# Kernel tuning notes

Hardware: AMD Instinct MI355X
Metric: run time of the kernel (lower is better)

Reference implementation:

```python
import jax, jax.numpy as jnp
import numpy as np

NUM_NODES = 100000
NODE_FEAT_DIM = 512
EDGE_FEAT_DIM = 512
MEM_DIM = NODE_FEAT_DIM + EDGE_FEAT_DIM  # 1024
BATCH = 65536


def setup_inputs() -> dict:
    key = jax.random.key(0)
    k_ids, k_mem, k_emb, kq, ks, kk = jax.random.split(key, 6)
    scale = 1.0 / np.sqrt(MEM_DIM)
    inp = {
        "node_ids": jax.random.randint(k_ids, (BATCH,), 0, NUM_NODES, dtype=jnp.int64)
        if jax.config.jax_enable_x64 else
        jax.random.randint(k_ids, (BATCH,), 0, NUM_NODES, dtype=jnp.int32),
        # memory bank: (N, 1, D); randomized (instead of the zero init) so math is non-trivial
        "node_memories": jax.random.normal(k_mem, (NUM_NODES, 1, MEM_DIM), dtype=jnp.float32) * 0.02,
        "node_embedding": jax.random.normal(k_emb, (NUM_NODES, MEM_DIM), dtype=jnp.float32) * 0.02,
        "Wq": jax.random.normal(jax.random.fold_in(kq, 0), (MEM_DIM, NODE_FEAT_DIM), dtype=jnp.float32) * scale,
        "bq": jnp.zeros((NODE_FEAT_DIM,), dtype=jnp.float32),
        "Ws": jax.random.normal(jax.random.fold_in(ks, 0), (MEM_DIM, NODE_FEAT_DIM), dtype=jnp.float32) * scale,
        "bs": jnp.zeros((NODE_FEAT_DIM,), dtype=jnp.float32),
        "Wk": jax.random.normal(jax.random.fold_in(kk, 0), (MEM_DIM, NODE_FEAT_DIM), dtype=jnp.float32) * scale,
        "bk": jnp.zeros((NODE_FEAT_DIM,), dtype=jnp.float32),
    }
    return inp


def reference(node_ids, node_memories, node_embedding, Wq, bq, Ws, bs, Wk, bk):
    ids = node_ids.astype(jnp.int32)
    # torch.sum(node_memories[ids], dim=2): reduces feature dim -> (B, 1)
    mem_sum = jnp.sum(node_memories[ids], axis=2)          # (B, 1)
    x = mem_sum + node_embedding[ids]                      # broadcast -> (B, D)
    q = jax.nn.sigmoid(x @ Wq + bq)                        # (B, node_feat_dim)
    s = jax.nn.sigmoid(x @ Ws + bs)
    k = jax.nn.sigmoid(x @ Wk + bk)
    return (q, s, k)
```

## Files before the change

### kernel.cpp

```cpp
#include <hip/hip_runtime.h>
#include <hip/hip_bf16.h>
#include <stdint.h>

#define BATCH_N 65536
#define KDIM 1024
#define NTOT 1536

typedef __bf16 bf16x8 __attribute__((ext_vector_type(8)));
typedef float f32x4 __attribute__((ext_vector_type(4)));

__device__ __forceinline__ unsigned short f2bf(float f) {
    unsigned u = __builtin_bit_cast(unsigned, f);
    u += 0x7FFFu + ((u >> 16) & 1u);
    return (unsigned short)(u >> 16);
}

__global__ __launch_bounds__(256) void prep_kernel(
    const int* __restrict__ ids,
    const float* __restrict__ mem,
    const float* __restrict__ emb,
    unsigned short* __restrict__ x)
{
    const int b    = blockIdx.x * 4 + (threadIdx.x >> 6);
    const int lane = threadIdx.x & 63;
    const int id   = ids[b];
    const float4* m4 = (const float4*)(mem + (size_t)id * KDIM) + lane;
    const float4* e4 = (const float4*)(emb + (size_t)id * KDIM) + lane;
    float4 v0 = m4[0];
    float4 v1 = m4[64];
    float4 v2 = m4[128];
    float4 v3 = m4[192];
    float s = (v0.x + v0.y + v0.z + v0.w) + (v1.x + v1.y + v1.z + v1.w)
            + (v2.x + v2.y + v2.z + v2.w) + (v3.x + v3.y + v3.z + v3.w);
    #pragma unroll
    for (int off = 1; off < 64; off <<= 1) s += __shfl_xor(s, off, 64);
    unsigned short* xb = x + (size_t)b * KDIM;
    #pragma unroll
    for (int q = 0; q < 4; ++q) {
        float4 e = e4[q * 64];
        ushort4 o;
        o.x = f2bf(s + e.x);
        o.y = f2bf(s + e.y);
        o.z = f2bf(s + e.z);
        o.w = f2bf(s + e.w);
        const int k   = q * 256 + lane * 4;
        const int ksw = k ^ ((b & 7) << 3);
        *(ushort4*)(xb + ksw) = o;
    }
}

__global__ __launch_bounds__(256) void wconv_kernel(
    const float* __restrict__ Wq, const float* __restrict__ Ws,
    const float* __restrict__ Wk, unsigned short* __restrict__ wt)
{
    const int gt = blockIdx.x * 256 + threadIdx.x;
    const int n  = gt % NTOT;
    const int kb = (gt / NTOT) * 4;
    const float* W = (n < 512) ? Wq : ((n < 1024) ? Ws : Wk);
    const int nn = n & 511;
    ushort4 o;
    o.x = f2bf(W[(size_t)(kb + 0) * 512 + nn]);
    o.y = f2bf(W[(size_t)(kb + 1) * 512 + nn]);
    o.z = f2bf(W[(size_t)(kb + 2) * 512 + nn]);
    o.w = f2bf(W[(size_t)(kb + 3) * 512 + nn]);
    const int ksw = kb ^ ((n & 7) << 3);
    *(ushort4*)(wt + (size_t)n * KDIM + ksw) = o;
}

#define BM 256
#define BN 256
#define BK 64
#define MT (BATCH_N / BM)
#define NT (NTOT / BN)
#define NWG (MT * NT)

#define BAR() asm volatile("s_barrier" ::: "memory")
#define VM4() asm volatile("s_waitcnt vmcnt(4)" ::: "memory")
#define VM0() asm volatile("s_waitcnt vmcnt(0)" ::: "memory")
#define AS1 __attribute__((address_space(1)))
#define AS3 __attribute__((address_space(3)))

__global__ __launch_bounds__(512, 2) void gemm_kernel(
    const unsigned short* __restrict__ X,
    const unsigned short* __restrict__ Wt,
    const float* __restrict__ bq, const float* __restrict__ bs,
    const float* __restrict__ bk, float* __restrict__ out)
{
    __shared__ __align__(16) unsigned short sA[32768];
    __shared__ __align__(16) unsigned short sB[32768];

    const int tid  = threadIdx.x;
    const int xcd  = blockIdx.x & 7;
    const int idx  = blockIdx.x >> 3;
    const int wgid = xcd * (NWG / 8) + idx;
    const int nt   = wgid % NT;
    const int mt   = wgid / NT;
    const int m0   = mt * BM;
    const int n0   = nt * BN;
    const int wid  = tid >> 6;
    const int lane = tid & 63;
    const int wm   = wid >> 2;
    const int wn   = wid & 3;
    const int r16  = lane & 15;
    const int kb0  = (lane >> 4) << 4;
    const int ksw  = (r16 & 7) << 4;

    f32x4 acc[8][4];
    #pragma unroll
    for (int i = 0; i < 8; i++)
        #pragma unroll
        for (int j = 0; j < 4; j++)
            acc[i][j] = f32x4{0.f, 0.f, 0.f, 0.f};

    bf16x8 af[4][2], bfr[4][2];

    const unsigned short* gA = X  + (size_t)(m0 + (tid >> 3)) * KDIM + (tid & 7) * 8;
    const unsigned short* gB = Wt + (size_t)(n0 + (tid >> 3)) * KDIM + (tid & 7) * 8;
    const int ldst = (tid & 448) * 8;

#define STAGE_A(slot, kt) do {                                                  \
    _Pragma("unroll")                                                            \
    for (int h = 0; h < 2; ++h)                                                  \
        _Pragma("unroll")                                                        \
        for (int c = 0; c < 2; ++c)                                              \
            __builtin_amdgcn_global_load_lds(                                    \
                (const AS1 void*)(gA + (size_t)(h * 128 + c * 64) * KDIM + (kt) * BK), \
                (AS3 void*)(&sA[(slot) * 16384 + h * 8192 + c * 4096 + ldst]),   \
                16, 0, 0);                                                       \
} while (0)
#define STAGE_B(slot, kt) do {                                                  \
    _Pragma("unroll")                                                            \
    for (int h = 0; h < 2; ++h)                                                  \
        _Pragma("unroll")                                                        \
        for (int c = 0; c < 2; ++c)                                              \
            __builtin_amdgcn_global_load_lds(                                    \
                (const AS1 void*)(gB + (size_t)(h * 128 + c * 64) * KDIM + (kt) * BK), \
                (AS3 void*)(&sB[(slot) * 16384 + h * 8192 + c * 4096 + ldst]),   \
                16, 0, 0);                                                       \
} while (0)

#define RD_A(slot, qa) do {                                                     \
    const char* p = (const char*)&sA[(slot) * 16384 + (qa) * 8192];              \
    _Pragma("unroll")                                                            \
    for (int i = 0; i < 4; ++i)                                                  \
        _Pragma("unroll")                                                        \
        for (int kk = 0; kk < 2; ++kk)                                           \
            af[i][kk] = *(const bf16x8*)(p + (wm * 64 + i * 16 + r16) * 128      \
                                           + ((kk * 64 + kb0) ^ ksw));           \
} while (0)
#define RD_B(slot) do {                                                         \
    const char* p = (const char*)&sB[(slot) * 16384 + (wn >> 1) * 8192];         \
    _Pragma("unroll")                                                            \
    for (int j = 0; j < 4; ++j)                                                  \
        _Pragma("unroll")                                                        \
        for (int kk = 0; kk < 2; ++kk)                                           \
            bfr[j][kk] = *(const bf16x8*)(p + ((wn & 1) * 64 + j * 16 + r16) * 128 \
                                            + ((kk * 64 + kb0) ^ ksw));          \
} while (0)

#define MM(QA) do {                                                             \
    __builtin_amdgcn_s_setprio(1);                                               \
    _Pragma("unroll")                                                            \
    for (int i = 0; i < 4; ++i)                                                  \
        _Pragma("unroll")                                                        \
        for (int j = 0; j < 4; ++j)                                              \
            _Pragma("unroll")                                                    \
            for (int kk = 0; kk < 2; ++kk)                                       \
                acc[(QA) * 4 + i][j] = __builtin_amdgcn_mfma_f32_16x16x32_bf16(  \
                    af[i][kk], bfr[j][kk], acc[(QA) * 4 + i][j], 0, 0, 0);       \
    __builtin_amdgcn_s_setprio(0);                                               \
} while (0)

    STAGE_A(0, 0); STAGE_B(0, 0); STAGE_A(1, 1);
    VM4();
    BAR();
    RD_A(0, 0); RD_B(0);

    #pragma unroll 1
    for (int t = 0; t < 14; ++t) {
        const int s = t & 1, s1 = s ^ 1;
        BAR();
        MM(0);
        RD_A(s, 1);
        STAGE_B(s1, t + 1);
        BAR();
        MM(1);
        STAGE_A(s, t + 2);
        VM4();
        BAR();
        RD_A(s1, 0); RD_B(s1);
    }
    BAR(); MM(0); RD_A(0, 1); STAGE_B(1, 15);
    BAR(); MM(1); VM0();
    BAR(); RD_A(1, 0); RD_B(1);
    BAR(); MM(0); RD_A(1, 1);
    BAR(); MM(1);

    const int grp = nt >> 1;
    const float* bias = (grp == 0) ? bq : ((grp == 1) ? bs : bk);
    float* obase = out + (size_t)grp * ((size_t)BATCH_N * 512);
    const int cb = (nt & 1) * 256;
    #pragma unroll
    for (int j = 0; j < 4; ++j) {
        const int col = cb + wn * 64 + j * 16 + r16;
        const float bv = bias[col];
        #pragma unroll
        for (int qa = 0; qa < 2; ++qa)
            #pragma unroll
            for (int i = 0; i < 4; ++i) {
                const int rbase = m0 + qa * 128 + wm * 64 + i * 16 + ((lane >> 4) << 2);
                #pragma unroll
                for (int r = 0; r < 4; ++r) {
                    float v = acc[qa * 4 + i][j][r] + bv;
                    v = 1.0f / (1.0f + __expf(-v));
                    __builtin_nontemporal_store(v, &obase[(size_t)(rbase + r) * 512 + col]);
                }
            }
    }
#undef STAGE_A
#undef STAGE_B
#undef RD_A
#undef RD_B
#undef MM
}

extern "C" void kernel_launch(void* const* d_in, const int* in_sizes, int n_in,
                              void* d_out, int out_size, void* d_ws, size_t ws_size,
                              hipStream_t stream) {
    const int*   ids = (const int*)d_in[0];
    const float* mem = (const float*)d_in[1];
    const float* emb = (const float*)d_in[2];
    const float* Wq  = (const float*)d_in[3];
    const float* bq  = (const float*)d_in[4];
    const float* Ws  = (const float*)d_in[5];
    const float* bs  = (const float*)d_in[6];
    const float* Wk  = (const float*)d_in[7];
    const float* bk  = (const float*)d_in[8];
    float* out = (float*)d_out;

    unsigned short* x  = (unsigned short*)d_ws;
    unsigned short* wt = x + (size_t)BATCH_N * KDIM;

    hipLaunchKernelGGL(wconv_kernel, dim3(NTOT), dim3(256), 0, stream, Wq, Ws, Wk, wt);
    hipLaunchKernelGGL(prep_kernel, dim3(BATCH_N / 4), dim3(256), 0, stream, ids, mem, emb, x);
    hipLaunchKernelGGL(gemm_kernel, dim3(NWG), dim3(512), 0, stream,
                       x, wt, bq, bs, bk, out);
}
```

Baseline: 412.0 us.

## Replace LDS-staged GEMM with direct global-to-register fragment loads on smaller tiles

```diff
diff --git a/kernel.cpp b/kernel.cpp
--- a/kernel.cpp
+++ b/kernel.cpp
@@ -43,9 +43,7 @@
         o.y = f2bf(s + e.y);
         o.z = f2bf(s + e.z);
         o.w = f2bf(s + e.w);
-        const int k   = q * 256 + lane * 4;
-        const int ksw = k ^ ((b & 7) << 3);
-        *(ushort4*)(xb + ksw) = o;
+        *(ushort4*)(xb + q * 256 + lane * 4) = o;
     }
 }
 
@@ -63,32 +61,21 @@
     o.y = f2bf(W[(size_t)(kb + 1) * 512 + nn]);
     o.z = f2bf(W[(size_t)(kb + 2) * 512 + nn]);
     o.w = f2bf(W[(size_t)(kb + 3) * 512 + nn]);
-    const int ksw = kb ^ ((n & 7) << 3);
-    *(ushort4*)(wt + (size_t)n * KDIM + ksw) = o;
+    *(ushort4*)(wt + (size_t)n * KDIM + kb) = o;
 }
 
-#define BM 256
-#define BN 256
-#define BK 64
+#define BM 128
+#define BN 128
 #define MT (BATCH_N / BM)
 #define NT (NTOT / BN)
 #define NWG (MT * NT)
 
-#define BAR() asm volatile("s_barrier" ::: "memory")
-#define VM4() asm volatile("s_waitcnt vmcnt(4)" ::: "memory")
-#define VM0() asm volatile("s_waitcnt vmcnt(0)" ::: "memory")
-#define AS1 __attribute__((address_space(1)))
-#define AS3 __attribute__((address_space(3)))
-
-__global__ __launch_bounds__(512, 2) void gemm_kernel(
+__global__ __launch_bounds__(256, 2) void gemm_kernel(
     const unsigned short* __restrict__ X,
     const unsigned short* __restrict__ Wt,
     const float* __restrict__ bq, const float* __restrict__ bs,
     const float* __restrict__ bk, float* __restrict__ out)
 {
-    __shared__ __align__(16) unsigned short sA[32768];
-    __shared__ __align__(16) unsigned short sB[32768];
-
     const int tid  = threadIdx.x;
     const int xcd  = blockIdx.x & 7;
     const int idx  = blockIdx.x >> 3;
@@ -99,128 +86,80 @@
     const int n0   = nt * BN;
     const int wid  = tid >> 6;
     const int lane = tid & 63;
-    const int wm   = wid >> 2;
-    const int wn   = wid & 3;
+    const int wm   = wid >> 1;
+    const int wn   = wid & 1;
     const int r16  = lane & 15;
-    const int kb0  = (lane >> 4) << 4;
-    const int ksw  = (r16 & 7) << 4;
+    const int kc8  = (lane >> 4) << 3;
 
-    f32x4 acc[8][4];
+    const unsigned short* pA = X  + (size_t)(m0 + wm * 64 + r16) * KDIM + kc8;
+    const unsigned short* pB = Wt + (size_t)(n0 + wn * 64 + r16) * KDIM + kc8;
+
+    f32x4 acc[4][4];
     #pragma unroll
-    for (int i = 0; i < 8; i++)
+    for (int i = 0; i < 4; i++)
         #pragma unroll
         for (int j = 0; j < 4; j++)
             acc[i][j] = f32x4{0.f, 0.f, 0.f, 0.f};
 
-    bf16x8 af[4][2], bfr[4][2];
+    bf16x8 a0[4][2], b0[4][2], a1[4][2], b1[4][2];
 
-    const unsigned short* gA = X  + (size_t)(m0 + (tid >> 3)) * KDIM + (tid & 7) * 8;
-    const unsigned short* gB = Wt + (size_t)(n0 + (tid >> 3)) * KDIM + (tid & 7) * 8;
-    const int ldst = (tid & 448) * 8;
-
-#define STAGE_A(slot, kt) do {                                                  \
-    _Pragma("unroll")                                                            \
-    for (int h = 0; h < 2; ++h)                                                  \
-        _Pragma("unroll")                                                        \
-        for (int c = 0; c < 2; ++c)                                              \
-            __builtin_amdgcn_global_load_lds(                                    \
-                (const AS1 void*)(gA + (size_t)(h * 128 + c * 64) * KDIM + (kt) * BK), \
-                (AS3 void*)(&sA[(slot) * 16384 + h * 8192 + c * 4096 + ldst]),   \
-                16, 0, 0);                                                       \
-} while (0)
-#define STAGE_B(slot, kt) do {                                                  \
-    _Pragma("unroll")                                                            \
-    for (int h = 0; h < 2; ++h)                                                  \
-        _Pragma("unroll")                                                        \
-        for (int c = 0; c < 2; ++c)                                              \
-            __builtin_amdgcn_global_load_lds(                                    \
-                (const AS1 void*)(gB + (size_t)(h * 128 + c * 64) * KDIM + (kt) * BK), \
-                (AS3 void*)(&sB[(slot) * 16384 + h * 8192 + c * 4096 + ldst]),   \
-                16, 0, 0);                                                       \
-} while (0)
-
-#define RD_A(slot, qa) do {                                                     \
-    const char* p = (const char*)&sA[(slot) * 16384 + (qa) * 8192];              \
+#define LOADA(SET, kt) do {                                                     \
     _Pragma("unroll")                                                            \
     for (int i = 0; i < 4; ++i)                                                  \
         _Pragma("unroll")                                                        \
         for (int kk = 0; kk < 2; ++kk)                                           \
-            af[i][kk] = *(const bf16x8*)(p + (wm * 64 + i * 16 + r16) * 128      \
-                                           + ((kk * 64 + kb0) ^ ksw));           \
+            SET[i][kk] = *(const bf16x8*)(pA + (size_t)i * 16 * KDIM             \
+                                             + (kt) * 64 + kk * 32);             \
 } while (0)
-#define RD_B(slot) do {                                                         \
-    const char* p = (const char*)&sB[(slot) * 16384 + (wn >> 1) * 8192];         \
+#define LOADB(SET, kt) do {                                                     \
     _Pragma("unroll")                                                            \
     for (int j = 0; j < 4; ++j)                                                  \
         _Pragma("unroll")                                                        \
         for (int kk = 0; kk < 2; ++kk)                                           \
-            bfr[j][kk] = *(const bf16x8*)(p + ((wn & 1) * 64 + j * 16 + r16) * 128 \
-                                            + ((kk * 64 + kb0) ^ ksw));          \
+            SET[j][kk] = *(const bf16x8*)(pB + (size_t)j * 16 * KDIM             \
+                                             + (kt) * 64 + kk * 32);             \
 } while (0)
-
-#define MM(QA) do {                                                             \
-    __builtin_amdgcn_s_setprio(1);                                               \
+#define MM(SA, SB) do {                                                         \
     _Pragma("unroll")                                                            \
     for (int i = 0; i < 4; ++i)                                                  \
         _Pragma("unroll")                                                        \
         for (int j = 0; j < 4; ++j)                                              \
             _Pragma("unroll")                                                    \
             for (int kk = 0; kk < 2; ++kk)                                       \
-                acc[(QA) * 4 + i][j] = __builtin_amdgcn_mfma_f32_16x16x32_bf16(  \
-                    af[i][kk], bfr[j][kk], acc[(QA) * 4 + i][j], 0, 0, 0);       \
-    __builtin_amdgcn_s_setprio(0);                                               \
+                acc[i][j] = __builtin_amdgcn_mfma_f32_16x16x32_bf16(             \
+                    SA[i][kk], SB[j][kk], acc[i][j], 0, 0, 0);                   \
 } while (0)
 
-    STAGE_A(0, 0); STAGE_B(0, 0); STAGE_A(1, 1);
-    VM4();
-    BAR();
-    RD_A(0, 0); RD_B(0);
+    LOADA(a0, 0); LOADB(b0, 0);
+    #pragma unroll
+    for (int t = 0; t < 16; t += 2) {
+        if (t + 1 < 16) { LOADA(a1, t + 1); LOADB(b1, t + 1); }
+        MM(a0, b0);
+        if (t + 2 < 16) { LOADA(a0, t + 2); LOADB(b0, t + 2); }
+        if (t + 1 < 16) { MM(a1, b1); }
+    }
 
-    #pragma unroll 1
-    for (int t = 0; t < 14; ++t) {
-        const int s = t & 1, s1 = s ^ 1;
-        BAR();
-        MM(0);
-        RD_A(s, 1);
-        STAGE_B(s1, t + 1);
-        BAR();
-        MM(1);
-        STAGE_A(s, t + 2);
-        VM4();
-        BAR();
-        RD_A(s1, 0); RD_B(s1);
-    }
-    BAR(); MM(0); RD_A(0, 1); STAGE_B(1, 15);
-    BAR(); MM(1); VM0();
-    BAR(); RD_A(1, 0); RD_B(1);
-    BAR(); MM(0); RD_A(1, 1);
-    BAR(); MM(1);
-
-    const int grp = nt >> 1;
+    const int grp = n0 >> 9;
     const float* bias = (grp == 0) ? bq : ((grp == 1) ? bs : bk);
     float* obase = out + (size_t)grp * ((size_t)BATCH_N * 512);
-    const int cb = (nt & 1) * 256;
+    const int nb = n0 & 511;
     #pragma unroll
     for (int j = 0; j < 4; ++j) {
-        const int col = cb + wn * 64 + j * 16 + r16;
+        const int col = nb + wn * 64 + j * 16 + r16;
         const float bv = bias[col];
         #pragma unroll
-        for (int qa = 0; qa < 2; ++qa)
+        for (int i = 0; i < 4; ++i) {
+            const int rbase = m0 + wm * 64 + i * 16 + ((lane >> 4) << 2);
             #pragma unroll
-            for (int i = 0; i < 4; ++i) {
-                const int rbase = m0 + qa * 128 + wm * 64 + i * 16 + ((lane >> 4) << 2);
-                #pragma unroll
-                for (int r = 0; r < 4; ++r) {
-                    float v = acc[qa * 4 + i][j][r] + bv;
-                    v = 1.0f / (1.0f + __expf(-v));
-                    __builtin_nontemporal_store(v, &obase[(size_t)(rbase + r) * 512 + col]);
-                }
+            for (int r = 0; r < 4; ++r) {
+                float v = acc[i][j][r] + bv;
+                v = 1.0f / (1.0f + __expf(-v));
+                __builtin_nontemporal_store(v, &obase[(size_t)(rbase + r) * 512 + col]);
             }
+        }
     }
-#undef STAGE_A
-#undef STAGE_B
-#undef RD_A
-#undef RD_B
+#undef LOADA
+#undef LOADB
 #undef MM
 }
 
@@ -243,6 +182,6 @@
 
     hipLaunchKernelGGL(wconv_kernel, dim3(NTOT), dim3(256), 0, stream, Wq, Ws, Wk, wt);
     hipLaunchKernelGGL(prep_kernel, dim3(BATCH_N / 4), dim3(256), 0, stream, ids, mem, emb, x);
-    hipLaunchKernelGGL(gemm_kernel, dim3(NWG), dim3(512), 0, stream,
+    hipLaunchKernelGGL(gemm_kernel, dim3(NWG), dim3(256), 0, stream,
                        x, wt, bq, bs, bk, out);
 }
```

New measurement: 864.1 us. +109.8%, slower.
